# Kernel tuning notes

Measured on AMD Instinct MI355X. Metric: run time of the kernel, lower is better.

Reference implementation:

```python
import jax, jax.numpy as jnp
import numpy as np

B, N, D_FEAT = 16, 4096, 64
NPOINT, NSAMPLE = 1024, 32
MLP = [64, 64, 128]
IN_CH = 3 + D_FEAT
EPS = 1e-5  # BatchNorm eps (torch default)


def _fps(xyz, npoint):
    # Farthest point sampling; sequential scan over npoint steps (matches torch loop).
    b, n, _ = xyz.shape
    def step(carry, _):
        distance, farthest = carry  # (B,N) running min dist, (B,) current centroid idx
        centroid = jnp.take_along_axis(xyz, farthest[:, None, None], axis=1)  # (B,1,3)
        d = jnp.sum((xyz - centroid) ** 2, -1)  # (B,N)
        distance = jnp.minimum(distance, d)
        nxt = jnp.argmax(distance, -1).astype(jnp.int32)
        return (distance, nxt), farthest
    init = (jnp.full((b, n), jnp.inf, dtype=xyz.dtype),
            jnp.full((b,), n // 2, dtype=jnp.int32))
    _, centroids = jax.lax.scan(step, init, None, length=npoint)
    return centroids.T  # (B, npoint)


def _gather(pts, idx):
    # pts: (B,N,C); idx: (B,...) int -> (B,...,C)
    return jax.vmap(lambda p, i: p[i])(pts, idx)


def setup_inputs() -> dict:
    key = jax.random.key(0)
    ks = jax.random.split(key, 16)
    inp = {
        'xyz': jax.random.normal(ks[0], (B, N, 3), jnp.float32),
        'points': jax.random.normal(ks[1], (B, N, D_FEAT), jnp.float32),
    }
    last = IN_CH
    for li, oc in enumerate(MLP):
        inp[f'W{li}'] = jax.random.normal(ks[2 + li], (oc, last), jnp.float32) * (1.0 / np.sqrt(last))
        inp[f'b{li}'] = jnp.zeros((oc,), jnp.float32)
        inp[f'g{li}'] = jnp.ones((oc,), jnp.float32)
        inp[f'be{li}'] = jnp.zeros((oc,), jnp.float32)
        last = oc
    C = MLP[-1]; R = C // 8
    inp['aW1'] = jax.random.normal(ks[10], (R, C), jnp.float32) * (1.0 / np.sqrt(C))
    inp['aW2'] = jax.random.normal(ks[11], (C, R), jnp.float32) * (1.0 / np.sqrt(R))
    return inp


def reference(xyz, points, W0, b0, g0, be0, W1, b1, g1, be1, W2, b2, g2, be2, aW1, aW2):
    fps_idx = _fps(xyz, NPOINT)                 # (B,S) int32
    new_xyz = _gather(xyz, fps_idx)             # (B,S,3)
    # squared distances (B,S,N) via matmul expansion (as torch square_distance)
    d = (-2.0 * jnp.einsum('bsc,bnc->bsn', new_xyz, xyz)
         + jnp.sum(new_xyz ** 2, -1)[..., None]
         + jnp.sum(xyz ** 2, -1)[:, None, :])
    _, idx = jax.lax.top_k(-d, NSAMPLE)         # (B,S,k) nearest neighbors
    grouped_xyz = _gather(xyz, idx)             # (B,S,k,3)
    rel = grouped_xyz - new_xyz[:, :, None, :]  # relative coords
    feat = _gather(points, idx)                 # (B,S,k,D)
    g = jnp.concatenate([rel, feat], axis=-1)   # (B,S,k,3+D) channels-last
    # 1x1 conv MLP + BatchNorm (training-mode batch stats) + ReLU
    for (W, b, ga, be) in ((W0, b0, g0, be0), (W1, b1, g1, be1), (W2, b2, g2, be2)):
        g = jnp.einsum('bskc,oc->bsko', g, W) + b
        mu = g.mean(axis=(0, 1, 2))
        var = g.var(axis=(0, 1, 2))
        g = ga * (g - mu) * jax.lax.rsqrt(var + EPS) + be
        g = jax.nn.relu(g)
    new_points = g.max(axis=2)                  # max over nsample -> (B,S,C)
    # channel attention on (B,C,S) == reductions over S here
    avg = new_points.mean(axis=1)               # (B,C)
    mx = new_points.max(axis=1)                 # (B,C)
    def fc(v):
        return jnp.einsum('cr,br->bc', aW2, jax.nn.relu(jnp.einsum('rc,bc->br', aW1, v)))
    scale = jax.nn.sigmoid(fc(avg) + fc(mx))    # (B,C)
    new_points = new_points * scale[:, None, :]
    return new_xyz, new_points, fps_idx
```

## Files before the change

### kernel.cpp

```cpp
#include <hip/hip_runtime.h>
#include <hip/hip_bf16.h>

#define BB 16
#define NN 4096
#define SS 1024
#define KS 32
#define DF 64
#define INC 67
#define C1 64
#define C2 64
#define C3 128
#define ROWS (BB*SS*KS)
#define EPSBN 1e-5f
#define F_INF (__builtin_inff())

typedef __bf16 bf16;
typedef __bf16 bfrag __attribute__((ext_vector_type(8)));
typedef float  ffrag __attribute__((ext_vector_type(4)));
typedef float  f2    __attribute__((ext_vector_type(2)));
typedef unsigned long long u64;

#define OUT_NXYZ 0
#define OUT_NP   49152
#define OUT_FPS  2146304

#define OFF_FPS   0u
#define OFF_NXYZ  65536u
#define OFF_IDX   262144u
#define OFF_STATS 2359296u
#define OFF_ASUM  2555904u
#define OFF_AMAX  2621440u
#define OFF_BNC   2686976u
#define OFF_SCALE 2690048u
#define OFF_NP0   2698240u
#define OFF_YMAX  11086848u
#define OFF_H1    19475456u
#define OFF_H2    86584320u
#define ZERO_BYTES (196608u + 65536u + 65536u)

#define DPP_MAX_STEP(k, ctrl, rmask, bc) { \
  int _lo = __builtin_amdgcn_update_dpp(0, (int)(unsigned)(k), (ctrl), (rmask), 0xf, (bc)); \
  int _hi = __builtin_amdgcn_update_dpp(0, (int)((k)>>32),     (ctrl), (rmask), 0xf, (bc)); \
  u64 _k2 = ((u64)(unsigned)_hi << 32) | (unsigned)_lo; \
  if (_k2 > (k)) (k) = _k2; }

__device__ __forceinline__ u64 dpp_wavemax64(u64 k){
  DPP_MAX_STEP(k, 0x111, 0xf, true)
  DPP_MAX_STEP(k, 0x112, 0xf, true)
  DPP_MAX_STEP(k, 0x114, 0xf, true)
  DPP_MAX_STEP(k, 0x118, 0xf, true)
  DPP_MAX_STEP(k, 0x142, 0xa, false)
  DPP_MAX_STEP(k, 0x143, 0xc, false)
  return k;
}

__device__ __forceinline__ u64 bcast63(u64 k){
  unsigned lo = (unsigned)__builtin_amdgcn_readlane((int)(unsigned)k, 63);
  unsigned hi = (unsigned)__builtin_amdgcn_readlane((int)(k>>32), 63);
  return ((u64)hi<<32) | lo;
}

__global__ __launch_bounds__(512) void fps_kernel(const float* __restrict__ xyz,
                                                  int* __restrict__ fps_i,
                                                  float* __restrict__ nxyz_ws,
                                                  float* __restrict__ out)
{
  #pragma clang fp contract(off)
  __shared__ float lx[NN], ly[NN], lz[NN];
  __shared__ int lfps[SS];
  __shared__ u64 slotk[2][8];
  int b = blockIdx.x, t = threadIdx.x;
  const float* xb = xyz + (size_t)b*NN*3;
  for (int p = t; p < NN; p += 512){ lx[p]=xb[p*3]; ly[p]=xb[p*3+1]; lz[p]=xb[p*3+2]; }
  __syncthreads();
  f2 px2[4], py2[4], pz2[4], pd2[4];
  int p0 = t*8;
  #pragma unroll
  for (int j=0;j<4;++j){
    px2[j] = (f2){lx[p0+2*j], lx[p0+2*j+1]};
    py2[j] = (f2){ly[p0+2*j], ly[p0+2*j+1]};
    pz2[j] = (f2){lz[p0+2*j], lz[p0+2*j+1]};
    pd2[j] = (f2){F_INF, F_INF};
  }
  float cx = lx[NN/2], cy = ly[NN/2], cz = lz[NN/2];
  if (t==0) lfps[0]=NN/2;
  int wv = t >> 6, lane = t & 63;
  for (int it=1; it<SS; ++it){
    f2 c2x = (f2){cx,cx}, c2y = (f2){cy,cy}, c2z = (f2){cz,cz};
    float bv=-1.f; int bi=p0;
    #pragma unroll
    for (int j=0;j<4;++j){
      f2 dx = px2[j]-c2x, dy = py2[j]-c2y, dz = pz2[j]-c2z;
      f2 d = (dx*dx + dy*dy) + dz*dz;
      f2 nd = (f2){fminf(pd2[j].x, d.x), fminf(pd2[j].y, d.y)};
      pd2[j]=nd;
      if (nd.x > bv){ bv=nd.x; bi=p0+2*j; }
      if (nd.y > bv){ bv=nd.y; bi=p0+2*j+1; }
    }
    u64 key = ((u64)__float_as_uint(bv) << 32) | (unsigned)(~bi);
    key = dpp_wavemax64(key);
    key = bcast63(key);
    int p = it & 1;
    if (lane == 0) slotk[p][wv] = key;
    __syncthreads();
    u64 k = slotk[p][t & 7];
    DPP_MAX_STEP(k, 0xB1, 0xf, true)
    DPP_MAX_STEP(k, 0x4E, 0xf, true)
    DPP_MAX_STEP(k, 0x141, 0xf, true)
    int i = ~(unsigned)k;
    cx = lx[i]; cy = ly[i]; cz = lz[i];
    if (t==0) lfps[it]=i;
  }
  __syncthreads();
  for (int s=t; s<SS; s+=512){
    int i = lfps[s];
    fps_i[b*SS+s]=i;
    out[OUT_FPS + b*SS + s] = (float)i;
    float xx=lx[i], yy=ly[i], zz=lz[i];
    int o3 = (b*SS+s)*3;
    out[OUT_NXYZ+o3]=xx; out[OUT_NXYZ+o3+1]=yy; out[OUT_NXYZ+o3+2]=zz;
    nxyz_ws[o3]=xx; nxyz_ws[o3+1]=yy; nxyz_ws[o3+2]=zz;
  }
}

__global__ __launch_bounds__(64) void knn_kernel(const float* __restrict__ xyz,
                                                 const float* __restrict__ nxyz,
                                                 int* __restrict__ knn)
{
  __shared__ float ld[NN];
  int lane = threadIdx.x;
  int bs = blockIdx.x;
  int b = bs >> 10;
  const float* xb = xyz + (size_t)b*NN*3;
  float sx=nxyz[bs*3], sy=nxyz[bs*3+1], sz=nxyz[bs*3+2];
  float gv[8]; int gi[8];
  float lv = F_INF; int li = 0;
  #pragma unroll
  for (int g=0; g<8; ++g){
    float bgv = F_INF; int bgi = 0;
    #pragma unroll
    for (int jj=0; jj<8; ++jj){
      int p = (g*8+jj)*64 + lane;
      float dx=xb[p*3]-sx, dy=xb[p*3+1]-sy, dz=xb[p*3+2]-sz;
      float d = dx*dx+dy*dy+dz*dz;
      ld[p] = d;
      if (d < bgv){ bgv=d; bgi=p; }
    }
    gv[g]=bgv; gi[g]=bgi;
    if (bgv < lv){ lv=bgv; li=bgi; }
  }
  int kept = 0;
  for (int it=0; it<KS; ++it){
    u64 mk = ~(((u64)__float_as_uint(lv) << 32) | (unsigned)li);
    mk = dpp_wavemax64(mk);
    mk = bcast63(mk);
    int i = (int)(unsigned)(~mk);
    if (lane==it) kept = i;
    if ((i & 63) == lane){
      int j = i >> 6;
      ld[i] = F_INF;
      int g = j >> 3;
      float bgv=F_INF; int bgi=0;
      for (int jj=0;jj<8;++jj){
        int p = (g*8+jj)*64 + lane;
        float d = ld[p];
        if (d<bgv){bgv=d;bgi=p;}
      }
      #pragma unroll
      for (int q=0;q<8;++q){ if (q==g){ gv[q]=bgv; gi[q]=bgi; } }
      lv=F_INF; li=0;
      #pragma unroll
      for (int q=0;q<8;++q){ if (gv[q]<lv){ lv=gv[q]; li=gi[q]; } }
    }
  }
  if (lane < KS) knn[bs*KS + lane] = kept;
}

__global__ __launch_bounds__(256) void conv1_kernel(const float* __restrict__ xyz,
                                                    const float* __restrict__ points,
                                                    const float* __restrict__ W0,
                                                    const float* __restrict__ b0,
                                                    const float* __restrict__ nxyz,
                                                    const int* __restrict__ knn,
                                                    bf16* __restrict__ h1,
                                                    float* __restrict__ stats)
{
  __shared__ __align__(16) bf16 As[64][104];
  __shared__ __align__(16) bf16 Bs[64][104];
  __shared__ float s1[C1], s2[C1];
  int t = threadIdx.x;
  int Rbase = blockIdx.x * 64;
  if (t < C1){ s1[t]=0.f; s2[t]=0.f; }
  {
    int o = t >> 2, q = t & 3;
    const float* wr = W0 + o*INC;
    for (int cc = q*24; cc < q*24+24; ++cc){
      float w;
      if (cc < 64) w = wr[3+cc];
      else if (cc < 67) w = wr[cc-64];
      else w = 0.f;
      Bs[o][cc] = (bf16)w;
    }
  }
  {
    int r = t >> 2, q = t & 3;
    int R = Rbase + r;
    int bs = R >> 5;
    int bIdx = bs >> 10;
    int nI = knn[R];
    const float* pr = points + ((size_t)(bIdx*NN + nI))*DF + q*16;
    float4 f0 = *(const float4*)(pr);
    float4 f1 = *(const float4*)(pr+4);
    float4 f2v = *(const float4*)(pr+8);
    float4 f3 = *(const float4*)(pr+12);
    bf16* ap = &As[r][q*16];
    ap[0]=(bf16)f0.x; ap[1]=(bf16)f0.y; ap[2]=(bf16)f0.z; ap[3]=(bf16)f0.w;
    ap[4]=(bf16)f1.x; ap[5]=(bf16)f1.y; ap[6]=(bf16)f1.z; ap[7]=(bf16)f1.w;
    ap[8]=(bf16)f2v.x; ap[9]=(bf16)f2v.y; ap[10]=(bf16)f2v.z; ap[11]=(bf16)f2v.w;
    ap[12]=(bf16)f3.x; ap[13]=(bf16)f3.y; ap[14]=(bf16)f3.z; ap[15]=(bf16)f3.w;
    if (q==0){
      const float* xr = xyz + ((size_t)(bIdx*NN + nI))*3;
      const float* nr = nxyz + bs*3;
      As[r][64]=(bf16)(xr[0]-nr[0]);
      As[r][65]=(bf16)(xr[1]-nr[1]);
      As[r][66]=(bf16)(xr[2]-nr[2]);
      for (int cc=67; cc<96; ++cc) As[r][cc]=(bf16)0.f;
    }
  }
  __syncthreads();
  int wv = t >> 6, lane = t & 63;
  int row16 = wv * 16;
  int arow = lane & 15, kgrp = lane >> 4;
  ffrag acc[4] = {};
  #pragma unroll
  for (int kc = 0; kc < 3; ++kc){
    bfrag af = *(const bfrag*)&As[row16 + arow][kc*32 + kgrp*8];
    #pragma unroll
    for (int nt = 0; nt < 4; ++nt){
      bfrag bfv = *(const bfrag*)&Bs[nt*16 + arow][kc*32 + kgrp*8];
      acc[nt] = __builtin_amdgcn_mfma_f32_16x16x32_bf16(af, bfv, acc[nt], 0,0,0);
    }
  }
  #pragma unroll
  for (int nt=0; nt<4; ++nt){
    int c = nt*16 + arow;
    float bias = b0[c];
    float ls1=0.f, ls2=0.f;
    #pragma unroll
    for (int r=0;r<4;++r){
      float y = acc[nt][r] + bias;
      int grow = Rbase + row16 + kgrp*4 + r;
      h1[(size_t)grow*C1 + c] = (bf16)y;
      ls1 += y; ls2 += y*y;
    }
    ls1 += __shfl_xor(ls1, 16); ls1 += __shfl_xor(ls1, 32);
    ls2 += __shfl_xor(ls2, 16); ls2 += __shfl_xor(ls2, 32);
    if (kgrp==0){ atomicAdd(&s1[c], ls1); atomicAdd(&s2[c], ls2); }
  }
  __syncthreads();
  if (t < C1){
    float* gp = stats + (blockIdx.x & 63)*256;
    atomicAdd(&gp[t], s1[t]);
    atomicAdd(&gp[128 + t], s2[t]);
  }
}

__global__ void bnfin_kernel(const float* __restrict__ stats, const float* __restrict__ g,
                             const float* __restrict__ be, float* __restrict__ bnc, int C)
{
  int c = threadIdx.x; if (c >= C) return;
  float a1=0.f, a2=0.f;
  for (int q=0;q<64;++q){ a1 += stats[q*256+c]; a2 += stats[q*256+128+c]; }
  float inv = 1.f/(float)ROWS;
  float mu = a1*inv; float var = a2*inv - mu*mu;
  float a = g[c]*rsqrtf(var + EPSBN);
  bnc[c] = a; bnc[128+c] = be[c] - mu*a;
}

__global__ __launch_bounds__(256) void conv2_kernel(const bf16* __restrict__ h1,
                                                    const float* __restrict__ W1,
                                                    const float* __restrict__ b1,
                                                    const float* __restrict__ bnc,
                                                    bf16* __restrict__ h2,
                                                    float* __restrict__ stats)
{
  __shared__ __align__(16) bf16 As[64][72];
  __shared__ __align__(16) bf16 Bs[64][72];
  __shared__ float s1[C2], s2[C2];
  int t = threadIdx.x;
  int Rbase = blockIdx.x * 64;
  if (t < C2){ s1[t]=0.f; s2[t]=0.f; }
  {
    int o = t >> 2, q = t & 3;
    const float* wr = W1 + o*64 + q*16;
    bf16* bp = &Bs[o][q*16];
    #pragma unroll
    for (int v=0; v<4; ++v){
      float4 f = *(const float4*)(wr + v*4);
      bp[v*4+0]=(bf16)f.x; bp[v*4+1]=(bf16)f.y; bp[v*4+2]=(bf16)f.z; bp[v*4+3]=(bf16)f.w;
    }
  }
  {
    int r = t >> 2, q = t & 3;
    int R = Rbase + r;
    const bf16* hr = h1 + (size_t)R*64 + q*16;
    bfrag h0 = *(const bfrag*)hr;
    bfrag h1v = *(const bfrag*)(hr+8);
    #pragma unroll
    for (int j=0;j<8;++j){
      int c=q*16+j;
      As[r][c] = (bf16)fmaxf(fmaf(bnc[c], (float)h0[j], bnc[128+c]), 0.f);
    }
    #pragma unroll
    for (int j=0;j<8;++j){
      int c=q*16+8+j;
      As[r][c] = (bf16)fmaxf(fmaf(bnc[c], (float)h1v[j], bnc[128+c]), 0.f);
    }
  }
  __syncthreads();
  int wv = t >> 6, lane = t & 63;
  int row16 = wv * 16;
  int arow = lane & 15, kgrp = lane >> 4;
  ffrag acc[4] = {};
  #pragma unroll
  for (int kc = 0; kc < 2; ++kc){
    bfrag af = *(const bfrag*)&As[row16 + arow][kc*32 + kgrp*8];
    #pragma unroll
    for (int nt = 0; nt < 4; ++nt){
      bfrag bfv = *(const bfrag*)&Bs[nt*16 + arow][kc*32 + kgrp*8];
      acc[nt] = __builtin_amdgcn_mfma_f32_16x16x32_bf16(af, bfv, acc[nt], 0,0,0);
    }
  }
  #pragma unroll
  for (int nt=0; nt<4; ++nt){
    int c = nt*16 + arow;
    float bias = b1[c];
    float ls1=0.f, ls2=0.f;
    #pragma unroll
    for (int r=0;r<4;++r){
      float y = acc[nt][r] + bias;
      int grow = Rbase + row16 + kgrp*4 + r;
      h2[(size_t)grow*C2 + c] = (bf16)y;
      ls1 += y; ls2 += y*y;
    }
    ls1 += __shfl_xor(ls1, 16); ls1 += __shfl_xor(ls1, 32);
    ls2 += __shfl_xor(ls2, 16); ls2 += __shfl_xor(ls2, 32);
    if (kgrp==0){ atomicAdd(&s1[c], ls1); atomicAdd(&s2[c], ls2); }
  }
  __syncthreads();
  if (t < C2){
    float* gp = stats + (blockIdx.x & 63)*256;
    atomicAdd(&gp[t], s1[t]);
    atomicAdd(&gp[128 + t], s2[t]);
  }
}

__global__ __launch_bounds__(256) void conv3_kernel(const bf16* __restrict__ h2,
                                                    const float* __restrict__ W2,
                                                    const float* __restrict__ b2,
                                                    const float* __restrict__ bnc,
                                                    float* __restrict__ ymax,
                                                    float* __restrict__ stats)
{
  __shared__ __align__(16) bf16 As[64][72];
  __shared__ __align__(16) bf16 Bs[128][72];
  __shared__ float s1[C3], s2[C3];
  __shared__ float wmax[4][C3];
  int t = threadIdx.x;
  int Rbase = blockIdx.x * 64;
  if (t < C3){ s1[t]=0.f; s2[t]=0.f; }
  {
    int o = t >> 1, q = t & 1;
    const float* wr = W2 + o*64 + q*32;
    bf16* bp = &Bs[o][q*32];
    #pragma unroll
    for (int v=0; v<8; ++v){
      float4 f = *(const float4*)(wr + v*4);
      bp[v*4+0]=(bf16)f.x; bp[v*4+1]=(bf16)f.y; bp[v*4+2]=(bf16)f.z; bp[v*4+3]=(bf16)f.w;
    }
  }
  {
    int r = t >> 2, q = t & 3;
    int R = Rbase + r;
    const bf16* hr = h2 + (size_t)R*64 + q*16;
    bfrag h0 = *(const bfrag*)hr;
    bfrag h1v = *(const bfrag*)(hr+8);
    #pragma unroll
    for (int j=0;j<8;++j){
      int c=q*16+j;
      As[r][c] = (bf16)fmaxf(fmaf(bnc[c], (float)h0[j], bnc[128+c]), 0.f);
    }
    #pragma unroll
    for (int j=0;j<8;++j){
      int c=q*16+8+j;
      As[r][c] = (bf16)fmaxf(fmaf(bnc[c], (float)h1v[j], bnc[128+c]), 0.f);
    }
  }
  __syncthreads();
  int wv = t >> 6, lane = t & 63;
  int row16 = wv * 16;
  int arow = lane & 15, kgrp = lane >> 4;
  ffrag acc[8] = {};
  #pragma unroll
  for (int kc = 0; kc < 2; ++kc){
    bfrag af = *(const bfrag*)&As[row16 + arow][kc*32 + kgrp*8];
    #pragma unroll
    for (int nt = 0; nt < 8; ++nt){
      bfrag bfv = *(const bfrag*)&Bs[nt*16 + arow][kc*32 + kgrp*8];
      acc[nt] = __builtin_amdgcn_mfma_f32_16x16x32_bf16(af, bfv, acc[nt], 0,0,0);
    }
  }
  #pragma unroll
  for (int nt=0; nt<8; ++nt){
    int c = nt*16 + arow;
    float bias = b2[c];
    float ls1=0.f, ls2=0.f, mm=-F_INF;
    #pragma unroll
    for (int r=0;r<4;++r){
      float y = acc[nt][r] + bias;
      ls1 += y; ls2 += y*y; mm = fmaxf(mm, y);
    }
    ls1 += __shfl_xor(ls1, 16); ls1 += __shfl_xor(ls1, 32);
    ls2 += __shfl_xor(ls2, 16); ls2 += __shfl_xor(ls2, 32);
    mm = fmaxf(mm, __shfl_xor(mm, 16)); mm = fmaxf(mm, __shfl_xor(mm, 32));
    if (kgrp==0){ atomicAdd(&s1[c], ls1); atomicAdd(&s2[c], ls2); wmax[wv][c]=mm; }
  }
  __syncthreads();
  {
    int half = t >> 7;
    int c = t & 127;
    float m = fmaxf(wmax[half*2][c], wmax[half*2+1][c]);
    ymax[(size_t)(blockIdx.x*2 + half)*C3 + c] = m;
  }
  if (t < C3){
    float* gp = stats + (blockIdx.x & 63)*256;
    atomicAdd(&gp[t], s1[t]);
    atomicAdd(&gp[128 + t], s2[t]);
  }
}

__global__ __launch_bounds__(256) void attreduce_kernel(const float* __restrict__ ymax,
                                                        const float* __restrict__ bnc,
                                                        float* __restrict__ np0,
                                                        float* __restrict__ asum,
                                                        unsigned* __restrict__ amax)
{
  __shared__ float rs[256], rm[256];
  int t = threadIdx.x;
  int b = blockIdx.x >> 3, sg = blockIdx.x & 7;
  int c = t & 127, h = t >> 7;
  float a = bnc[c], bb = bnc[128+c];
  size_t base = ((size_t)(b*1024 + sg*128 + h*64))*128 + c;
  float s = 0.f, m = 0.f;
  #pragma unroll 4
  for (int j=0;j<64;++j){
    float v = fmaxf(fmaf(a, ymax[base + (size_t)j*128], bb), 0.f);
    np0[base + (size_t)j*128] = v;
    s += v; m = fmaxf(m, v);
  }
  rs[t]=s; rm[t]=m;
  __syncthreads();
  if (t < 128){
    float s2 = rs[t] + rs[t+128];
    float m2 = fmaxf(rm[t], rm[t+128]);
    atomicAdd(&asum[b*128+t], s2);
    atomicMax(&amax[b*128+t], __float_as_uint(m2));
  }
}

__global__ __launch_bounds__(256) void attn_kernel(const float* __restrict__ asum,
                                                   const unsigned* __restrict__ amax,
                                                   const float* __restrict__ aW1,
                                                   const float* __restrict__ aW2,
                                                   float* __restrict__ scale)
{
  __shared__ float avg[16][128], mx[16][128], hA[16][16], hM[16][16];
  int t = threadIdx.x;
  for (int i=t; i<2048; i+=256){
    int b=i>>7, c=i&127;
    avg[b][c]=asum[i]*(1.f/1024.f); mx[b][c]=__uint_as_float(amax[i]);
  }
  __syncthreads();
  {
    int b=t>>4, r=t&15;
    float sa=0.f, sm=0.f;
    for (int c=0;c<128;++c){ float w=aW1[r*128+c]; sa+=w*avg[b][c]; sm+=w*mx[b][c]; }
    hA[b][r]=fmaxf(sa,0.f); hM[b][r]=fmaxf(sm,0.f);
  }
  __syncthreads();
  for (int i=t;i<2048;i+=256){
    int b=i>>7,c=i&127;
    float o=0.f;
    for (int r=0;r<16;++r){ o += aW2[c*16+r]*(hA[b][r]+hM[b][r]); }
    scale[i] = 1.f/(1.f+expf(-o));
  }
}

__global__ __launch_bounds__(256) void finout_kernel(const float* __restrict__ np0,
                                                     const float* __restrict__ scale,
                                                     float* __restrict__ out)
{
  int i = blockIdx.x*256 + threadIdx.x;
  int c = i & 127; int b = i >> 17;
  out[OUT_NP + i] = np0[i] * scale[b*128+c];
}

extern "C" void kernel_launch(void* const* d_in, const int* in_sizes, int n_in,
                              void* d_out, int out_size, void* d_ws, size_t ws_size,
                              hipStream_t stream)
{
  const float* xyz    = (const float*)d_in[0];
  const float* points = (const float*)d_in[1];
  const float* W0 = (const float*)d_in[2];
  const float* b0 = (const float*)d_in[3];
  const float* g0 = (const float*)d_in[4];
  const float* be0= (const float*)d_in[5];
  const float* W1 = (const float*)d_in[6];
  const float* b1 = (const float*)d_in[7];
  const float* g1 = (const float*)d_in[8];
  const float* be1= (const float*)d_in[9];
  const float* W2 = (const float*)d_in[10];
  const float* b2 = (const float*)d_in[11];
  const float* g2 = (const float*)d_in[12];
  const float* be2= (const float*)d_in[13];
  const float* aW1= (const float*)d_in[14];
  const float* aW2= (const float*)d_in[15];
  float* out = (float*)d_out;
  char* ws = (char*)d_ws;

  int*      fpsI  = (int*)(ws + OFF_FPS);
  float*    nxyz  = (float*)(ws + OFF_NXYZ);
  int*      knnI  = (int*)(ws + OFF_IDX);
  float*    stats = (float*)(ws + OFF_STATS);
  float*    asum  = (float*)(ws + OFF_ASUM);
  unsigned* amax  = (unsigned*)(ws + OFF_AMAX);
  float*    bnc   = (float*)(ws + OFF_BNC);
  float*    scl   = (float*)(ws + OFF_SCALE);
  float*    np0   = (float*)(ws + OFF_NP0);
  float*    ymax  = (float*)(ws + OFF_YMAX);
  bf16*     h1    = (bf16*)(ws + OFF_H1);
  bf16*     h2    = (bf16*)(ws + OFF_H2);

  hipMemsetAsync(ws + OFF_STATS, 0, ZERO_BYTES, stream);
  fps_kernel<<<BB, 512, 0, stream>>>(xyz, fpsI, nxyz, out);
  knn_kernel<<<BB*SS, 64, 0, stream>>>(xyz, nxyz, knnI);
  conv1_kernel<<<ROWS/64, 256, 0, stream>>>(xyz, points, W0, b0, nxyz, knnI, h1, stats);
  bnfin_kernel<<<1, 128, 0, stream>>>(stats, g0, be0, bnc, C1);
  conv2_kernel<<<ROWS/64, 256, 0, stream>>>(h1, W1, b1, bnc, h2, stats + 64*256);
  bnfin_kernel<<<1, 128, 0, stream>>>(stats + 64*256, g1, be1, bnc + 256, C2);
  conv3_kernel<<<ROWS/64, 256, 0, stream>>>(h2, W2, b2, bnc + 256, ymax, stats + 2*64*256);
  bnfin_kernel<<<1, 128, 0, stream>>>(stats + 2*64*256, g2, be2, bnc + 512, C3);
  attreduce_kernel<<<BB*8, 256, 0, stream>>>(ymax, bnc + 512, np0, asum, amax);
  attn_kernel<<<1, 256, 0, stream>>>(asum, amax, aW1, aW2, scl);
  finout_kernel<<<(BB*SS*C3)/256, 256, 0, stream>>>(np0, scl, out);
}
```

Before: 1.160 ms.

## Shrink FPS block to 256 threads and split argmax into value then index reductions

```diff
diff --git a/kernel.cpp b/kernel.cpp
--- a/kernel.cpp
+++ b/kernel.cpp
@@ -44,6 +44,26 @@
   u64 _k2 = ((u64)(unsigned)_hi << 32) | (unsigned)_lo; \
   if (_k2 > (k)) (k) = _k2; }
 
+#define DPP_FMAX_STEP(v, ctrl, rmask) { \
+  int _s = __builtin_amdgcn_update_dpp(0, __float_as_int(v), (ctrl), (rmask), 0xf, true); \
+  v = fmaxf(v, __int_as_float(_s)); }
+
+#define DPP_UMAX_STEP(v, ctrl, rmask) { \
+  unsigned _s = (unsigned)__builtin_amdgcn_update_dpp(0, (int)(v), (ctrl), (rmask), 0xf, true); \
+  if (_s > (v)) (v) = _s; }
+
+__device__ __forceinline__ float dpp_wavemax_f32(float v){
+  DPP_FMAX_STEP(v, 0x111, 0xf) DPP_FMAX_STEP(v, 0x112, 0xf)
+  DPP_FMAX_STEP(v, 0x114, 0xf) DPP_FMAX_STEP(v, 0x118, 0xf)
+  DPP_FMAX_STEP(v, 0x142, 0xa) DPP_FMAX_STEP(v, 0x143, 0xc)
+  return v;
+}
+__device__ __forceinline__ unsigned dpp_wavemax_u32(unsigned v){
+  DPP_UMAX_STEP(v, 0x111, 0xf) DPP_UMAX_STEP(v, 0x112, 0xf)
+  DPP_UMAX_STEP(v, 0x114, 0xf) DPP_UMAX_STEP(v, 0x118, 0xf)
+  DPP_UMAX_STEP(v, 0x142, 0xa) DPP_UMAX_STEP(v, 0x143, 0xc)
+  return v;
+}
 __device__ __forceinline__ u64 dpp_wavemax64(u64 k){
   DPP_MAX_STEP(k, 0x111, 0xf, true)
   DPP_MAX_STEP(k, 0x112, 0xf, true)
@@ -53,14 +73,13 @@
   DPP_MAX_STEP(k, 0x143, 0xc, false)
   return k;
 }
-
 __device__ __forceinline__ u64 bcast63(u64 k){
   unsigned lo = (unsigned)__builtin_amdgcn_readlane((int)(unsigned)k, 63);
   unsigned hi = (unsigned)__builtin_amdgcn_readlane((int)(k>>32), 63);
   return ((u64)hi<<32) | lo;
 }
 
-__global__ __launch_bounds__(512) void fps_kernel(const float* __restrict__ xyz,
+__global__ __launch_bounds__(256) void fps_kernel(const float* __restrict__ xyz,
                                                   int* __restrict__ fps_i,
                                                   float* __restrict__ nxyz_ws,
                                                   float* __restrict__ out)
@@ -68,15 +87,15 @@
   #pragma clang fp contract(off)
   __shared__ float lx[NN], ly[NN], lz[NN];
   __shared__ int lfps[SS];
-  __shared__ u64 slotk[2][8];
+  __shared__ u64 slotk[2][4];
   int b = blockIdx.x, t = threadIdx.x;
   const float* xb = xyz + (size_t)b*NN*3;
-  for (int p = t; p < NN; p += 512){ lx[p]=xb[p*3]; ly[p]=xb[p*3+1]; lz[p]=xb[p*3+2]; }
-  __syncthreads();
-  f2 px2[4], py2[4], pz2[4], pd2[4];
-  int p0 = t*8;
-  #pragma unroll
-  for (int j=0;j<4;++j){
+  for (int p = t; p < NN; p += 256){ lx[p]=xb[p*3]; ly[p]=xb[p*3+1]; lz[p]=xb[p*3+2]; }
+  __syncthreads();
+  f2 px2[8], py2[8], pz2[8], pd2[8];
+  int p0 = t*16;
+  #pragma unroll
+  for (int j=0;j<8;++j){
     px2[j] = (f2){lx[p0+2*j], lx[p0+2*j+1]};
     py2[j] = (f2){ly[p0+2*j], ly[p0+2*j+1]};
     pz2[j] = (f2){lz[p0+2*j], lz[p0+2*j+1]};
@@ -87,32 +106,38 @@
   int wv = t >> 6, lane = t & 63;
   for (int it=1; it<SS; ++it){
     f2 c2x = (f2){cx,cx}, c2y = (f2){cy,cy}, c2z = (f2){cz,cz};
-    float bv=-1.f; int bi=p0;
-    #pragma unroll
-    for (int j=0;j<4;++j){
+    f2 ma = (f2){-1.f,-1.f}, mb = (f2){-1.f,-1.f};
+    #pragma unroll
+    for (int j=0;j<8;++j){
       f2 dx = px2[j]-c2x, dy = py2[j]-c2y, dz = pz2[j]-c2z;
       f2 d = (dx*dx + dy*dy) + dz*dz;
       f2 nd = (f2){fminf(pd2[j].x, d.x), fminf(pd2[j].y, d.y)};
       pd2[j]=nd;
-      if (nd.x > bv){ bv=nd.x; bi=p0+2*j; }
-      if (nd.y > bv){ bv=nd.y; bi=p0+2*j+1; }
-    }
-    u64 key = ((u64)__float_as_uint(bv) << 32) | (unsigned)(~bi);
-    key = dpp_wavemax64(key);
-    key = bcast63(key);
+      if (j & 1){ mb = (f2){fmaxf(mb.x, nd.x), fmaxf(mb.y, nd.y)}; }
+      else      { ma = (f2){fmaxf(ma.x, nd.x), fmaxf(ma.y, nd.y)}; }
+    }
+    float wm = fmaxf(fmaxf(ma.x, ma.y), fmaxf(mb.x, mb.y));
+    float gv = dpp_wavemax_f32(wm);
+    gv = __int_as_float(__builtin_amdgcn_readlane(__float_as_int(gv), 63));
+    unsigned cand = 0xFFFFFFFFu;
+    #pragma unroll
+    for (int j=7;j>=0;--j){
+      if (pd2[j].y == gv) cand = (unsigned)(p0+2*j+1);
+      if (pd2[j].x == gv) cand = (unsigned)(p0+2*j);
+    }
+    unsigned nidx = dpp_wavemax_u32(~cand);
     int p = it & 1;
-    if (lane == 0) slotk[p][wv] = key;
+    if (lane == 63) slotk[p][wv] = ((u64)__float_as_uint(gv) << 32) | nidx;
     __syncthreads();
-    u64 k = slotk[p][t & 7];
+    u64 k = slotk[p][t & 3];
     DPP_MAX_STEP(k, 0xB1, 0xf, true)
     DPP_MAX_STEP(k, 0x4E, 0xf, true)
-    DPP_MAX_STEP(k, 0x141, 0xf, true)
     int i = ~(unsigned)k;
     cx = lx[i]; cy = ly[i]; cz = lz[i];
     if (t==0) lfps[it]=i;
   }
   __syncthreads();
-  for (int s=t; s<SS; s+=512){
+  for (int s=t; s<SS; s+=256){
     int i = lfps[s];
     fps_i[b*SS+s]=i;
     out[OUT_FPS + b*SS + s] = (float)i;
@@ -542,7 +567,7 @@
   bf16*     h2    = (bf16*)(ws + OFF_H2);
 
   hipMemsetAsync(ws + OFF_STATS, 0, ZERO_BYTES, stream);
-  fps_kernel<<<BB, 512, 0, stream>>>(xyz, fpsI, nxyz, out);
+  fps_kernel<<<BB, 256, 0, stream>>>(xyz, fpsI, nxyz, out);
   knn_kernel<<<BB*SS, 64, 0, stream>>>(xyz, nxyz, knnI);
   conv1_kernel<<<ROWS/64, 256, 0, stream>>>(xyz, points, W0, b0, nxyz, knnI, h1, stats);
   bnfin_kernel<<<1, 128, 0, stream>>>(stats, g0, be0, bnc, C1);
```

New measurement: 1.112 ms. 4.1% less time.
